# Kernel optimization log

Hardware: AMD Instinct MI355X
Metric: run time of the kernel (lower is better)

Reference implementation:

```python
import jax, jax.numpy as jnp
import numpy as np

NEG_SLOPE = 0.2  # PyG GATConv default leaky_relu slope
EPS = 1e-16


def gat_conv(x, src, dst, W, att_src, att_dst, bias, heads, concat):
    """PyG-style GATConv. x: [N, Fin]; W: [Fin, heads*C]; att_*: [heads, C].
    Edge (src j -> dst i): alpha_ij = softmax_i(leaky_relu(a_src.h_j + a_dst.h_i)).
    """
    N = x.shape[0]
    h = (x @ W).reshape(N, heads, -1)                       # [N, H, C]
    a_s = jnp.einsum('nhc,hc->nh', h, att_src)              # [N, H]
    a_d = jnp.einsum('nhc,hc->nh', h, att_dst)              # [N, H]
    e = jax.nn.leaky_relu(a_s[src] + a_d[dst], NEG_SLOPE)   # [E, H]
    # numerically stable segment softmax over incoming edges of each dst node
    e_max = jax.ops.segment_max(e, dst, num_segments=N)     # [N, H]
    e_max = jnp.where(jnp.isfinite(e_max), e_max, 0.0)      # isolated nodes
    ex = jnp.exp(e - e_max[dst])                            # [E, H]
    denom = jax.ops.segment_sum(ex, dst, num_segments=N)    # [N, H]
    alpha = ex / (denom[dst] + EPS)                         # [E, H]
    msg = alpha[:, :, None] * h[src]                        # [E, H, C]
    out = jax.ops.segment_sum(msg, dst, num_segments=N)     # [N, H, C]
    out = out.reshape(N, -1) if concat else out.mean(axis=1)
    return out + bias


def setup_inputs() -> dict:
    key = jax.random.key(0)
    ks = jax.random.split(key, 12)
    N, E = 100000, 1600000
    Fin, hidden, heads, Fout = 128, 128, 8, 64
    C1 = hidden // heads  # 16
    s = lambda f: 1.0 / np.sqrt(f)
    x = jax.random.normal(ks[0], (N, Fin), dtype=jnp.float32)
    edge_index = jax.random.randint(ks[1], (2, E), 0, N, dtype=jnp.int64)
    W1 = jax.random.normal(ks[2], (Fin, heads * C1), dtype=jnp.float32) * s(Fin)
    att_src1 = jax.random.normal(ks[3], (heads, C1), dtype=jnp.float32) * s(C1)
    att_dst1 = jax.random.normal(ks[4], (heads, C1), dtype=jnp.float32) * s(C1)
    b1 = jnp.zeros((hidden,), dtype=jnp.float32)
    W2 = jax.random.normal(ks[5], (hidden, Fout), dtype=jnp.float32) * s(hidden)
    att_src2 = jax.random.normal(ks[6], (1, Fout), dtype=jnp.float32) * s(Fout)
    att_dst2 = jax.random.normal(ks[7], (1, Fout), dtype=jnp.float32) * s(Fout)
    b2 = jnp.zeros((Fout,), dtype=jnp.float32)
    return {"x": x, "edge_index": edge_index,
            "W1": W1, "att_src1": att_src1, "att_dst1": att_dst1, "b1": b1,
            "W2": W2, "att_src2": att_src2, "att_dst2": att_dst2, "b2": b2}


def reference(x, edge_index, W1, att_src1, att_dst1, b1, W2, att_src2, att_dst2, b2):
    # eval mode: dropouts are identity
    src, dst = edge_index[0], edge_index[1]
    h = gat_conv(x, src, dst, W1, att_src1, att_dst1, b1, heads=8, concat=True)
    h = jax.nn.elu(h)
    out = gat_conv(h, src, dst, W2, att_src2, att_dst2, b2, heads=1, concat=False)
    return out
```

## Files before the change

### kernel.cpp

```cpp
#include <hip/hip_runtime.h>
#include <hip/hip_bf16.h>
#include <hip/hip_fp16.h>
#include <stdint.h>

#define SLOPE 0.2f
#define EPSV 1e-16f
#define LOG2E 1.44269504f
#define H1W 72
#define H2W 36

#define NPB2  256
#define NBLK  512

typedef __attribute__((ext_vector_type(8))) short bf16x8;
typedef __attribute__((ext_vector_type(4))) float f32x4;

static __device__ __forceinline__ uint32_t cvtpk(float a, float b) {
    uint32_t r;
    asm("v_cvt_pk_bf16_f32 %0, %1, %2" : "=v"(r) : "v"(a), "v"(b));
    return r;
}
static __device__ __forceinline__ float lof(uint32_t u) { return __uint_as_float(u << 16); }
static __device__ __forceinline__ float hif(uint32_t u) { return __uint_as_float(u & 0xffff0000u); }

static __device__ __forceinline__ uint32_t pkf16(float a, float b) {
    auto r = __builtin_amdgcn_cvt_pkrtz(a, b);
    return __builtin_bit_cast(uint32_t, r);
}

static __device__ __forceinline__ void fmix_lo(float& acc, uint32_t h2, float w) {
    asm("v_fma_mix_f32 %0, %1, %2, %0 op_sel_hi:[1,0,0]" : "+v"(acc) : "v"(h2), "v"(w));
}
static __device__ __forceinline__ void fmix_hi(float& acc, uint32_t h2, float w) {
    asm("v_fma_mix_f32 %0, %1, %2, %0 op_sel:[1,0,0] op_sel_hi:[1,0,0]" : "+v"(acc) : "v"(h2), "v"(w));
}

union FragCvt { uint4 u; bf16x8 f; };

__global__ __launch_bounds__(256) void prep_kernel(
    const float* __restrict__ W1, const float* __restrict__ W2,
    uint32_t* __restrict__ wt1hi, uint32_t* __restrict__ wt1lo,
    uint32_t* __restrict__ wt2hi, uint32_t* __restrict__ wt2lo)
{
    int t = threadIdx.x;
    if (blockIdx.x == 0) {
        for (int i = t; i < 128 * 64; i += 256) {
            int n = i >> 6, kp = i & 63;
            float w0 = W1[(2 * kp) * 128 + n], w1 = W1[(2 * kp + 1) * 128 + n];
            uint32_t h = cvtpk(w0, w1);
            wt1hi[n * 64 + kp] = h;
            wt1lo[n * 64 + kp] = cvtpk(w0 - lof(h), w1 - hif(h));
        }
    } else {
        for (int i = t; i < 64 * 64; i += 256) {
            int n = i >> 6, kp = i & 63;
            float w0 = W2[(2 * kp) * 64 + n], w1 = W2[(2 * kp + 1) * 64 + n];
            uint32_t h = cvtpk(w0, w1);
            wt2hi[n * 64 + kp] = h;
            wt2lo[n * 64 + kp] = cvtpk(w0 - lof(h), w1 - hif(h));
        }
    }
}

__global__ __launch_bounds__(256) void gemm1_mfma(
    const float* __restrict__ x,
    const uint32_t* __restrict__ wthi, const uint32_t* __restrict__ wtlo,
    const float* __restrict__ att_src, const float* __restrict__ att_dst,
    uint32_t* __restrict__ h1p, float* __restrict__ ad1, int N)
{
    __shared__ uint32_t lds[2][128 * 36];
    const int t = threadIdx.x;
    const int w = t >> 6, l = t & 63;
    const int cl = l & 15, rg = l >> 4;
    const int rowbase = blockIdx.x * 128 + w * 32;

    f32x4 zero = {0.f, 0.f, 0.f, 0.f};
    f32x4 acc[2][8];
    #pragma unroll
    for (int rt = 0; rt < 2; ++rt)
        #pragma unroll
        for (int tl = 0; tl < 8; ++tl) acc[rt][tl] = zero;

    for (int kh = 0; kh < 2; ++kh) {
        if (kh) __syncthreads();
        for (int i = t; i < 1024; i += 256) {
            int col = i >> 3, q = i & 7;
            *(uint4*)&lds[0][col * 36 + q * 4] = *(const uint4*)&wthi[col * 64 + kh * 32 + q * 4];
            *(uint4*)&lds[1][col * 36 + q * 4] = *(const uint4*)&wtlo[col * 64 + kh * 32 + q * 4];
        }
        __syncthreads();
        #pragma unroll
        for (int ks = 0; ks < 2; ++ks) {
            const int kg = kh * 64 + ks * 32 + rg * 8;
            bf16x8 ahi[2], alo[2];
            #pragma unroll
            for (int rt = 0; rt < 2; ++rt) {
                int row = rowbase + rt * 16 + cl;
                row = min(row, N - 1);
                const float* xr = x + (size_t)row * 128 + kg;
                float4 v0 = *(const float4*)xr;
                float4 v1 = *(const float4*)(xr + 4);
                uint32_t h0 = cvtpk(v0.x, v0.y), h1 = cvtpk(v0.z, v0.w);
                uint32_t h2 = cvtpk(v1.x, v1.y), h3 = cvtpk(v1.z, v1.w);
                uint32_t l0 = cvtpk(v0.x - lof(h0), v0.y - hif(h0));
                uint32_t l1 = cvtpk(v0.z - lof(h1), v0.w - hif(h1));
                uint32_t l2 = cvtpk(v1.x - lof(h2), v1.y - hif(h2));
                uint32_t l3 = cvtpk(v1.z - lof(h3), v1.w - hif(h3));
                FragCvt ch, clo;
                ch.u  = make_uint4(h0, h1, h2, h3);
                clo.u = make_uint4(l0, l1, l2, l3);
                ahi[rt] = ch.f; alo[rt] = clo.f;
            }
            #pragma unroll
            for (int tl = 0; tl < 8; ++tl) {
                const int off = (tl * 16 + cl) * 36 + ks * 16 + rg * 4;
                bf16x8 bhi = *(const bf16x8*)&lds[0][off];
                bf16x8 blo = *(const bf16x8*)&lds[1][off];
                #pragma unroll
                for (int rt = 0; rt < 2; ++rt) {
                    acc[rt][tl] = __builtin_amdgcn_mfma_f32_16x16x32_bf16(alo[rt], bhi, acc[rt][tl], 0, 0, 0);
                    acc[rt][tl] = __builtin_amdgcn_mfma_f32_16x16x32_bf16(ahi[rt], blo, acc[rt][tl], 0, 0, 0);
                    acc[rt][tl] = __builtin_amdgcn_mfma_f32_16x16x32_bf16(ahi[rt], bhi, acc[rt][tl], 0, 0, 0);
                }
            }
        }
    }

    #pragma unroll
    for (int rt = 0; rt < 2; ++rt) {
        const int rowb = rowbase + rt * 16 + rg * 4;
        #pragma unroll
        for (int tl = 0; tl < 8; ++tl) {
            f32x4 a = acc[rt][tl];
            float as_ = att_src[tl * 16 + cl] * LOG2E, ad_ = att_dst[tl * 16 + cl] * LOG2E;
            float s0 = a.x * as_, s1 = a.y * as_, s2 = a.z * as_, s3 = a.w * as_;
            float d0 = a.x * ad_, d1 = a.y * ad_, d2 = a.z * ad_, d3 = a.w * ad_;
            #pragma unroll
            for (int off = 1; off < 16; off <<= 1) {
                s0 += __shfl_xor(s0, off); s1 += __shfl_xor(s1, off);
                s2 += __shfl_xor(s2, off); s3 += __shfl_xor(s3, off);
                d0 += __shfl_xor(d0, off); d1 += __shfl_xor(d1, off);
                d2 += __shfl_xor(d2, off); d3 += __shfl_xor(d3, off);
            }
            float av[4] = {a.x, a.y, a.z, a.w};
            #pragma unroll
            for (int r = 0; r < 4; ++r) {
                float partner = __shfl_xor(av[r], 1);
                if (!(cl & 1)) {
                    int row = rowb + r;
                    if (row < N)
                        h1p[(size_t)row * H1W + tl * 8 + (cl >> 1)] = pkf16(av[r], partner);
                }
            }
            if (cl == 0) {
                float sv[4] = {s0, s1, s2, s3}, dv[4] = {d0, d1, d2, d3};
                #pragma unroll
                for (int r = 0; r < 4; ++r) {
                    int row = rowb + r;
                    if (row < N) {
                        h1p[(size_t)row * H1W + 64 + tl] = __float_as_uint(sv[r]);
                        ad1[row * 8 + tl] = dv[r];
                    }
                }
            }
        }
    }
}

__global__ __launch_bounds__(256) void gemm2_mfma(
    const float* __restrict__ h,
    const uint32_t* __restrict__ wthi, const uint32_t* __restrict__ wtlo,
    const float* __restrict__ att_src, const float* __restrict__ att_dst,
    uint32_t* __restrict__ h2p, float* __restrict__ ad2, int N)
{
    __shared__ uint32_t lds[2][64 * 36];
    const int t = threadIdx.x;
    const int w = t >> 6, l = t & 63;
    const int cl = l & 15, rg = l >> 4;
    const int rowbase = blockIdx.x * 128 + w * 32;

    f32x4 zero = {0.f, 0.f, 0.f, 0.f};
    f32x4 acc[2][4];
    #pragma unroll
    for (int rt = 0; rt < 2; ++rt)
        #pragma unroll
        for (int tl = 0; tl < 4; ++tl) acc[rt][tl] = zero;

    for (int kh = 0; kh < 2; ++kh) {
        if (kh) __syncthreads();
        for (int i = t; i < 512; i += 256) {
            int col = i >> 3, q = i & 7;
            *(uint4*)&lds[0][col * 36 + q * 4] = *(const uint4*)&wthi[col * 64 + kh * 32 + q * 4];
            *(uint4*)&lds[1][col * 36 + q * 4] = *(const uint4*)&wtlo[col * 64 + kh * 32 + q * 4];
        }
        __syncthreads();
        #pragma unroll
        for (int ks = 0; ks < 2; ++ks) {
            const int kg = kh * 64 + ks * 32 + rg * 8;
            bf16x8 ahi[2], alo[2];
            #pragma unroll
            for (int rt = 0; rt < 2; ++rt) {
                int row = rowbase + rt * 16 + cl;
                row = min(row, N - 1);
                const float* xr = h + (size_t)row * 128 + kg;
                float4 v0 = *(const float4*)xr;
                float4 v1 = *(const float4*)(xr + 4);
                uint32_t h0 = cvtpk(v0.x, v0.y), h1 = cvtpk(v0.z, v0.w);
                uint32_t h2 = cvtpk(v1.x, v1.y), h3 = cvtpk(v1.z, v1.w);
                uint32_t l0 = cvtpk(v0.x - lof(h0), v0.y - hif(h0));
                uint32_t l1 = cvtpk(v0.z - lof(h1), v0.w - hif(h1));
                uint32_t l2 = cvtpk(v1.x - lof(h2), v1.y - hif(h2));
                uint32_t l3 = cvtpk(v1.z - lof(h3), v1.w - hif(h3));
                FragCvt ch, clo;
                ch.u  = make_uint4(h0, h1, h2, h3);
                clo.u = make_uint4(l0, l1, l2, l3);
                ahi[rt] = ch.f; alo[rt] = clo.f;
            }
            #pragma unroll
            for (int tl = 0; tl < 4; ++tl) {
                const int off = (tl * 16 + cl) * 36 + ks * 16 + rg * 4;
                bf16x8 bhi = *(const bf16x8*)&lds[0][off];
                bf16x8 blo = *(const bf16x8*)&lds[1][off];
                #pragma unroll
                for (int rt = 0; rt < 2; ++rt) {
                    acc[rt][tl] = __builtin_amdgcn_mfma_f32_16x16x32_bf16(alo[rt], bhi, acc[rt][tl], 0, 0, 0);
                    acc[rt][tl] = __builtin_amdgcn_mfma_f32_16x16x32_bf16(ahi[rt], blo, acc[rt][tl], 0, 0, 0);
                    acc[rt][tl] = __builtin_amdgcn_mfma_f32_16x16x32_bf16(ahi[rt], bhi, acc[rt][tl], 0, 0, 0);
                }
            }
        }
    }

    #pragma unroll
    for (int rt = 0; rt < 2; ++rt) {
        const int rowb = rowbase + rt * 16 + rg * 4;
        float s0 = 0.f, s1 = 0.f, s2 = 0.f, s3 = 0.f;
        float d0 = 0.f, d1 = 0.f, d2 = 0.f, d3 = 0.f;
        #pragma unroll
        for (int tl = 0; tl < 4; ++tl) {
            f32x4 a = acc[rt][tl];
            float as_ = att_src[tl * 16 + cl] * LOG2E, ad_ = att_dst[tl * 16 + cl] * LOG2E;
            s0 += a.x * as_; s1 += a.y * as_; s2 += a.z * as_; s3 += a.w * as_;
            d0 += a.x * ad_; d1 += a.y * ad_; d2 += a.z * ad_; d3 += a.w * ad_;
            float av[4] = {a.x, a.y, a.z, a.w};
            #pragma unroll
            for (int r = 0; r < 4; ++r) {
                float partner = __shfl_xor(av[r], 1);
                if (!(cl & 1)) {
                    int row = rowb + r;
                    if (row < N)
                        h2p[(size_t)row * H2W + tl * 8 + (cl >> 1)] = pkf16(av[r], partner);
                }
            }
        }
        #pragma unroll
        for (int off = 1; off < 16; off <<= 1) {
            s0 += __shfl_xor(s0, off); s1 += __shfl_xor(s1, off);
            s2 += __shfl_xor(s2, off); s3 += __shfl_xor(s3, off);
            d0 += __shfl_xor(d0, off); d1 += __shfl_xor(d1, off);
            d2 += __shfl_xor(d2, off); d3 += __shfl_xor(d3, off);
        }
        if (cl == 0) {
            float sv[4] = {s0, s1, s2, s3}, dv[4] = {d0, d1, d2, d3};
            #pragma unroll
            for (int r = 0; r < 4; ++r) {
                int row = rowb + r;
                if (row < N) {
                    h2p[(size_t)row * H2W + 32] = __float_as_uint(sv[r]);
                    ad2[row] = dv[r];
                }
            }
        }
    }
}

__global__ __launch_bounds__(256) void s_count(
    const int* __restrict__ ei, int* __restrict__ pbh, int E, int NB, int chunk)
{
    __shared__ int hist[512];
    int t = threadIdx.x;
    hist[t] = 0; hist[t + 256] = 0;
    __syncthreads();
    int e0 = blockIdx.x * chunk, e1 = min(E, e0 + chunk);
    for (int e = e0 + t; e < e1; e += 256)
        atomicAdd(&hist[ei[E + e] >> 8], 1);
    __syncthreads();
    for (int b = t; b < NB; b += 256)
        pbh[(size_t)b * NBLK + blockIdx.x] = hist[b];
}

__global__ __launch_bounds__(256) void s_scanA(
    const int* __restrict__ pbh, int* __restrict__ btot, int NB)
{
    __shared__ int red[256];
    int b = blockIdx.x, t = threadIdx.x;
    int s = pbh[(size_t)b * NBLK + t] + pbh[(size_t)b * NBLK + 256 + t];
    red[t] = s; __syncthreads();
    for (int off = 128; off; off >>= 1) {
        if (t < off) red[t] += red[t + off];
        __syncthreads();
    }
    if (t == 0) btot[b] = red[0];
}

__global__ __launch_bounds__(512) void s_scanB(
    const int* __restrict__ btot, int* __restrict__ bucket_base, int NB, int E)
{
    __shared__ int sc[512];
    int t = threadIdx.x;
    int v = (t < NB) ? btot[t] : 0;
    sc[t] = v; __syncthreads();
    for (int off = 1; off < 512; off <<= 1) {
        int add = (t >= off) ? sc[t - off] : 0;
        __syncthreads();
        sc[t] += add;
        __syncthreads();
    }
    if (t < NB) bucket_base[t] = sc[t] - v;
    if (t == 0) bucket_base[NB] = E;
}

__global__ __launch_bounds__(256) void s_scanC(
    int* __restrict__ pbh, const int* __restrict__ bucket_base, int NB)
{
    __shared__ int ps[256];
    int b = blockIdx.x, t = threadIdx.x;
    int v0 = pbh[(size_t)b * NBLK + 2 * t], v1 = pbh[(size_t)b * NBLK + 2 * t + 1];
    int p = v0 + v1;
    ps[t] = p; __syncthreads();
    for (int off = 1; off < 256; off <<= 1) {
        int add = (t >= off) ? ps[t - off] : 0;
        __syncthreads();
        ps[t] += add;
        __syncthreads();
    }
    int ex = bucket_base[b] + ps[t] - p;
    pbh[(size_t)b * NBLK + 2 * t]     = ex;
    pbh[(size_t)b * NBLK + 2 * t + 1] = ex + v0;
}

__global__ __launch_bounds__(256) void s_place(
    const int* __restrict__ ei, const int* __restrict__ pbh,
    uint32_t* __restrict__ staging, int E, int NB, int chunk)
{
    __shared__ int lcur[512];
    int t = threadIdx.x;
    if (t < NB)       lcur[t]       = pbh[(size_t)t * NBLK + blockIdx.x];
    if (t + 256 < NB) lcur[t + 256] = pbh[(size_t)(t + 256) * NBLK + blockIdx.x];
    __syncthreads();
    int e0 = blockIdx.x * chunk, e1 = min(E, e0 + chunk);
    for (int e = e0 + t; e < e1; e += 256) {
        int s = ei[e], d = ei[E + e];
        int p = atomicAdd(&lcur[d >> 8], 1);
        staging[p] = ((uint32_t)s << 8) | (uint32_t)(d & 255);
    }
}

__global__ __launch_bounds__(256) void s_build(
    const uint32_t* __restrict__ staging, const int* __restrict__ bucket_base,
    int* __restrict__ row_start, int* __restrict__ sorted_src, int N, int E, int NB)
{
    __shared__ int cnt[256];
    __shared__ int ofs[256];
    __shared__ int ps[256];
    int b = blockIdx.x, t = threadIdx.x;
    int base = bucket_base[b], end = bucket_base[b + 1];
    cnt[t] = 0;
    __syncthreads();
    for (int i = base + t; i < end; i += 256)
        atomicAdd(&cnt[staging[i] & 255], 1);
    __syncthreads();
    int c = cnt[t];
    ps[t] = c; __syncthreads();
    for (int off = 1; off < 256; off <<= 1) {
        int add = (t >= off) ? ps[t - off] : 0;
        __syncthreads();
        ps[t] += add;
        __syncthreads();
    }
    int ex = ps[t] - c;
    ofs[t] = ex;
    int node = b * NPB2 + t;
    if (node < N) row_start[node] = base + ex;
    if (b == NB - 1 && t == 0) row_start[N] = E;
    __syncthreads();
    for (int i = base + t; i < end; i += 256) {
        uint32_t v = staging[i];
        int pos = base + atomicAdd(&ofs[v & 255], 1);
        sorted_src[pos] = (int)(v >> 8);
    }
}

__global__ __launch_bounds__(256) void gather1_kernel(
    const int* __restrict__ row_start, const int* __restrict__ sorted_src,
    const float* __restrict__ ad1, const uint32_t* __restrict__ h1p,
    const float* __restrict__ b1, float* __restrict__ hbuf, int N)
{
    int node = blockIdx.x * 4 + (threadIdx.x >> 6);
    if (node >= N) return;
    const int l  = threadIdx.x & 63;
    const int wh = l & 7;
    const int eA = l >> 3;
    const int c8 = l & 15;
    const int q  = l >> 4;
    const int hB = c8 >> 1;

    int r0 = row_start[node], r1 = row_start[node + 1];

    if (r0 == r1) {
        if (l < 16) {
            #pragma unroll
            for (int g = 0; g < 2; ++g) {
                float4 bv = *(const float4*)&b1[c8 * 8 + g * 4];
                bv.x = bv.x > 0.f ? bv.x : expm1f(bv.x);
                bv.y = bv.y > 0.f ? bv.y : expm1f(bv.y);
                bv.z = bv.z > 0.f ? bv.z : expm1f(bv.z);
                bv.w = bv.w > 0.f ? bv.w : expm1f(bv.w);
                *(float4*)&hbuf[(size_t)node * 128 + c8 * 8 + g * 4] = bv;
            }
        }
        return;
    }

    float adw = ad1[node * 8 + wh];
    const uint32_t* rowp = h1p + 4 * c8;
    float acc[8] = {0.f, 0.f, 0.f, 0.f, 0.f, 0.f, 0.f, 0.f};
    float den = 0.f;

    int jw = r0 + eA;
    int sw0 = sorted_src[jw < r1 ? jw : r0] * H1W;
    int j1 = r0 + 8 + eA;
    int sw1 = sorted_src[j1 < r1 ? j1 : r0] * H1W;
    float av0 = __uint_as_float(h1p[sw0 + 64 + wh]);

    for (int j = r0; j < r1; j += 8) {
        int jn = j + 16 + eA;
        int swn = sorted_src[jn < r1 ? jn : r0] * H1W;
        float avn = __uint_as_float(h1p[sw1 + 64 + wh]);

        float ev = av0 + adw;
        ev = ev > 0.f ? ev : SLOPE * ev;
        float w = (j + eA) < r1 ? exp2f(ev) : 0.f;
        den += w;

        #pragma unroll
        for (int k = 0; k < 2; ++k) {
            int eidx = q + 4 * k;
            float wk  = __shfl(w,   eidx * 8 + hB, 64);
            int   ofk = __shfl(sw0, eidx * 8,      64);
            uint4 hv = *(const uint4*)(rowp + ofk);
            fmix_lo(acc[0], hv.x, wk); fmix_hi(acc[1], hv.x, wk);
            fmix_lo(acc[2], hv.y, wk); fmix_hi(acc[3], hv.y, wk);
            fmix_lo(acc[4], hv.z, wk); fmix_hi(acc[5], hv.z, wk);
            fmix_lo(acc[6], hv.w, wk); fmix_hi(acc[7], hv.w, wk);
        }
        sw0 = sw1; sw1 = swn; av0 = avn;
    }

    den += __shfl_xor(den, 8, 64);
    den += __shfl_xor(den, 16, 64);
    den += __shfl_xor(den, 32, 64);
    float dB = __shfl(den, hB, 64);

    #pragma unroll
    for (int i = 0; i < 8; ++i) {
        acc[i] += __shfl_xor(acc[i], 16, 64);
        acc[i] += __shfl_xor(acc[i], 32, 64);
    }

    if (l < 16) {
        float inv = 1.0f / (dB + EPSV);
        #pragma unroll
        for (int g = 0; g < 2; ++g) {
            float4 bv = *(const float4*)&b1[c8 * 8 + g * 4];
            float v0 = acc[g * 4 + 0] * inv + bv.x;
            float v1 = acc[g * 4 + 1] * inv + bv.y;
            float v2 = acc[g * 4 + 2] * inv + bv.z;
            float v3 = acc[g * 4 + 3] * inv + bv.w;
            v0 = v0 > 0.f ? v0 : expm1f(v0);
            v1 = v1 > 0.f ? v1 : expm1f(v1);
            v2 = v2 > 0.f ? v2 : expm1f(v2);
            v3 = v3 > 0.f ? v3 : expm1f(v3);
            *(float4*)&hbuf[(size_t)node * 128 + c8 * 8 + g * 4] = make_float4(v0, v1, v2, v3);
        }
    }
}

__global__ __launch_bounds__(256) void gather2_kernel(
    const int* __restrict__ row_start, const int* __restrict__ sorted_src,
    const float* __restrict__ ad2, const uint32_t* __restrict__ h2p,
    const float* __restrict__ b2, float* __restrict__ out, int N)
{
    int node = blockIdx.x * 8 + (threadIdx.x >> 5);
    if (node >= N) return;
    const int l  = threadIdx.x & 31;
    const int eA = l & 7;
    const int c8 = l & 7;
    const int q  = l >> 3;

    int r0 = row_start[node], r1 = row_start[node + 1];

    if (r0 == r1) {
        if (l < 8) {
            #pragma unroll
            for (int g = 0; g < 2; ++g) {
                float4 bv = *(const float4*)&b2[c8 * 8 + g * 4];
                *(float4*)&out[(size_t)node * 64 + c8 * 8 + g * 4] = bv;
            }
        }
        return;
    }

    float ad = ad2[node];
    const uint32_t* rowp = h2p + 4 * c8;
    float acc[8] = {0.f, 0.f, 0.f, 0.f, 0.f, 0.f, 0.f, 0.f};
    float den = 0.f;

    int jw = r0 + eA;
    int sw0 = sorted_src[jw < r1 ? jw : r0] * H2W;
    int j1 = r0 + 8 + eA;
    int sw1 = sorted_src[j1 < r1 ? j1 : r0] * H2W;
    float av0 = __uint_as_float(h2p[sw0 + 32]);

    for (int j = r0; j < r1; j += 8) {
        int jn = j + 16 + eA;
        int swn = sorted_src[jn < r1 ? jn : r0] * H2W;
        float avn = __uint_as_float(h2p[sw1 + 32]);

        float ev = av0 + ad;
        ev = ev > 0.f ? ev : SLOPE * ev;
        float w = (j + eA) < r1 ? exp2f(ev) : 0.f;
        den += w;

        #pragma unroll
        for (int k = 0; k < 2; ++k) {
            int eidx = q + 4 * k;
            float wk  = __shfl(w,   eidx, 32);
            int   ofk = __shfl(sw0, eidx, 32);
            uint4 hv = *(const uint4*)(rowp + ofk);
            fmix_lo(acc[0], hv.x, wk); fmix_hi(acc[1], hv.x, wk);
            fmix_lo(acc[2], hv.y, wk); fmix_hi(acc[3], hv.y, wk);
            fmix_lo(acc[4], hv.z, wk); fmix_hi(acc[5], hv.z, wk);
            fmix_lo(acc[6], hv.w, wk); fmix_hi(acc[7], hv.w, wk);
        }
        sw0 = sw1; sw1 = swn; av0 = avn;
    }

    den += __shfl_xor(den, 1, 32);
    den += __shfl_xor(den, 2, 32);
    den += __shfl_xor(den, 4, 32);
    #pragma unroll
    for (int i = 0; i < 8; ++i) {
        acc[i] += __shfl_xor(acc[i], 8, 32);
        acc[i] += __shfl_xor(acc[i], 16, 32);
    }

    if (l < 8) {
        float inv = 1.0f / (den + EPSV);
        #pragma unroll
        for (int g = 0; g < 2; ++g) {
            float4 bv = *(const float4*)&b2[c8 * 8 + g * 4];
            *(float4*)&out[(size_t)node * 64 + c8 * 8 + g * 4] =
                make_float4(acc[g * 4 + 0] * inv + bv.x, acc[g * 4 + 1] * inv + bv.y,
                            acc[g * 4 + 2] * inv + bv.z, acc[g * 4 + 3] * inv + bv.w);
        }
    }
}

extern "C" void kernel_launch(void* const* d_in, const int* in_sizes, int n_in,
                              void* d_out, int out_size, void* d_ws, size_t ws_size,
                              hipStream_t stream)
{
    const int N = in_sizes[0] / 128;
    const int E = in_sizes[1] / 2;
    const int NB = (N + NPB2 - 1) / NPB2;
    const int chunk = (E + NBLK - 1) / NBLK;

    const float* x        = (const float*)d_in[0];
    const int*   ei       = (const int*)  d_in[1];
    const float* W1       = (const float*)d_in[2];
    const float* att_src1 = (const float*)d_in[3];
    const float* att_dst1 = (const float*)d_in[4];
    const float* b1       = (const float*)d_in[5];
    const float* W2       = (const float*)d_in[6];
    const float* att_src2 = (const float*)d_in[7];
    const float* att_dst2 = (const float*)d_in[8];
    const float* b2       = (const float*)d_in[9];
    float* out = (float*)d_out;

    uint32_t* h1p  = (uint32_t*)d_ws;
    float* hbuf    = (float*)(h1p + (size_t)N * H1W);
    float* ad1     = hbuf + (size_t)N * 128;
    float* ad2     = ad1  + (size_t)N * 8;
    int* row_start   = (int*)(ad2 + N);
    int* bucket_base = row_start + (N + 1);
    int* btot        = bucket_base + (NB + 1);
    int* pbh         = btot + NB;
    int* sorted_src  = pbh + (size_t)NB * NBLK;
    uint32_t* staging = (uint32_t*)(sorted_src + E);
    uint32_t* wt1hi = staging + E;
    uint32_t* wt1lo = wt1hi + 128 * 64;
    uint32_t* wt2hi = wt1lo + 128 * 64;
    uint32_t* wt2lo = wt2hi + 64 * 64;
    uint32_t* h2p   = h1p;

    prep_kernel<<<2, 256, 0, stream>>>(W1, W2, wt1hi, wt1lo, wt2hi, wt2lo);

    s_count<<<NBLK, 256, 0, stream>>>(ei, pbh, E, NB, chunk);
    s_scanA<<<NB, 256, 0, stream>>>(pbh, btot, NB);
    s_scanB<<<1, 512, 0, stream>>>(btot, bucket_base, NB, E);
    s_scanC<<<NB, 256, 0, stream>>>(pbh, bucket_base, NB);
    s_place<<<NBLK, 256, 0, stream>>>(ei, pbh, staging, E, NB, chunk);
    s_build<<<NB, 256, 0, stream>>>(staging, bucket_base, row_start, sorted_src, N, E, NB);

    gemm1_mfma<<<(N + 127) / 128, 256, 0, stream>>>(x, wt1hi, wt1lo, att_src1, att_dst1, h1p, ad1, N);
    gather1_kernel<<<(N + 3) / 4, 256, 0, stream>>>(row_start, sorted_src, ad1, h1p, b1, hbuf, N);

    gemm2_mfma<<<(N + 127) / 128, 256, 0, stream>>>(hbuf, wt2hi, wt2lo, att_src2, att_dst2, h2p, ad2, N);
    gather2_kernel<<<(N + 7) / 8, 256, 0, stream>>>(row_start, sorted_src, ad2, h2p, b2, out, N);
}
```

Before: 257.9 us.

## Fold weight prep and bucket scan into neighbours; software-pipeline gather row loads

Merges the weight-split prep kernel into s_count as two extra blocks and folds the single-block bucket scan into s_scanC, where each block recomputes the global prefix over bucket totals. Together these remove two kernel launches and their serialization gaps. Both gather kernels now issue the h-row loads for the next 8-edge group one iteration ahead, so gather latency overlaps the FMA work. The cost is redundant scan work in every s_scanC block and more registers held live in the gather loops.

```diff
diff --git a/kernel.cpp b/kernel.cpp
--- a/kernel.cpp
+++ b/kernel.cpp
@@ -36,31 +36,6 @@
 }
 
 union FragCvt { uint4 u; bf16x8 f; };
-
-__global__ __launch_bounds__(256) void prep_kernel(
-    const float* __restrict__ W1, const float* __restrict__ W2,
-    uint32_t* __restrict__ wt1hi, uint32_t* __restrict__ wt1lo,
-    uint32_t* __restrict__ wt2hi, uint32_t* __restrict__ wt2lo)
-{
-    int t = threadIdx.x;
-    if (blockIdx.x == 0) {
-        for (int i = t; i < 128 * 64; i += 256) {
-            int n = i >> 6, kp = i & 63;
-            float w0 = W1[(2 * kp) * 128 + n], w1 = W1[(2 * kp + 1) * 128 + n];
-            uint32_t h = cvtpk(w0, w1);
-            wt1hi[n * 64 + kp] = h;
-            wt1lo[n * 64 + kp] = cvtpk(w0 - lof(h), w1 - hif(h));
-        }
-    } else {
-        for (int i = t; i < 64 * 64; i += 256) {
-            int n = i >> 6, kp = i & 63;
-            float w0 = W2[(2 * kp) * 64 + n], w1 = W2[(2 * kp + 1) * 64 + n];
-            uint32_t h = cvtpk(w0, w1);
-            wt2hi[n * 64 + kp] = h;
-            wt2lo[n * 64 + kp] = cvtpk(w0 - lof(h), w1 - hif(h));
-        }
-    }
-}
 
 __global__ __launch_bounds__(256) void gemm1_mfma(
     const float* __restrict__ x,
@@ -275,10 +250,33 @@
 }
 
 __global__ __launch_bounds__(256) void s_count(
-    const int* __restrict__ ei, int* __restrict__ pbh, int E, int NB, int chunk)
-{
+    const int* __restrict__ ei, int* __restrict__ pbh, int E, int NB, int chunk,
+    const float* __restrict__ W1, const float* __restrict__ W2,
+    uint32_t* __restrict__ wt1hi, uint32_t* __restrict__ wt1lo,
+    uint32_t* __restrict__ wt2hi, uint32_t* __restrict__ wt2lo)
+{
+    int t = threadIdx.x;
+    if (blockIdx.x >= NBLK) {
+        if (blockIdx.x == NBLK) {
+            for (int i = t; i < 128 * 64; i += 256) {
+                int n = i >> 6, kp = i & 63;
+                float w0 = W1[(2 * kp) * 128 + n], w1 = W1[(2 * kp + 1) * 128 + n];
+                uint32_t h = cvtpk(w0, w1);
+                wt1hi[n * 64 + kp] = h;
+                wt1lo[n * 64 + kp] = cvtpk(w0 - lof(h), w1 - hif(h));
+            }
+        } else {
+            for (int i = t; i < 64 * 64; i += 256) {
+                int n = i >> 6, kp = i & 63;
+                float w0 = W2[(2 * kp) * 64 + n], w1 = W2[(2 * kp + 1) * 64 + n];
+                uint32_t h = cvtpk(w0, w1);
+                wt2hi[n * 64 + kp] = h;
+                wt2lo[n * 64 + kp] = cvtpk(w0 - lof(h), w1 - hif(h));
+            }
+        }
+        return;
+    }
     __shared__ int hist[512];
-    int t = threadIdx.x;
     hist[t] = 0; hist[t + 256] = 0;
     __syncthreads();
     int e0 = blockIdx.x * chunk, e1 = min(E, e0 + chunk);
@@ -303,29 +301,15 @@
     if (t == 0) btot[b] = red[0];
 }
 
-__global__ __launch_bounds__(512) void s_scanB(
-    const int* __restrict__ btot, int* __restrict__ bucket_base, int NB, int E)
-{
-    __shared__ int sc[512];
-    int t = threadIdx.x;
-    int v = (t < NB) ? btot[t] : 0;
-    sc[t] = v; __syncthreads();
-    for (int off = 1; off < 512; off <<= 1) {
-        int add = (t >= off) ? sc[t - off] : 0;
-        __syncthreads();
-        sc[t] += add;
-        __syncthreads();
-    }
-    if (t < NB) bucket_base[t] = sc[t] - v;
-    if (t == 0) bucket_base[NB] = E;
-}
-
 __global__ __launch_bounds__(256) void s_scanC(
-    int* __restrict__ pbh, const int* __restrict__ bucket_base, int NB)
+    int* __restrict__ pbh, const int* __restrict__ btot,
+    int* __restrict__ bucket_base, int NB, int E)
 {
     __shared__ int ps[256];
+    __shared__ int exv[512];
     int b = blockIdx.x, t = threadIdx.x;
-    int v0 = pbh[(size_t)b * NBLK + 2 * t], v1 = pbh[(size_t)b * NBLK + 2 * t + 1];
+    int v0 = (2 * t     < NB) ? btot[2 * t]     : 0;
+    int v1 = (2 * t + 1 < NB) ? btot[2 * t + 1] : 0;
     int p = v0 + v1;
     ps[t] = p; __syncthreads();
     for (int off = 1; off < 256; off <<= 1) {
@@ -334,9 +318,27 @@
         ps[t] += add;
         __syncthreads();
     }
-    int ex = bucket_base[b] + ps[t] - p;
+    int pex = ps[t] - p;
+    exv[2 * t] = pex; exv[2 * t + 1] = pex + v0;
+    __syncthreads();
+    int base = exv[b];
+    if (t == 0) {
+        bucket_base[b] = base;
+        if (b == NB - 1) bucket_base[NB] = E;
+    }
+    __syncthreads();
+    int w0 = pbh[(size_t)b * NBLK + 2 * t], w1 = pbh[(size_t)b * NBLK + 2 * t + 1];
+    int pp = w0 + w1;
+    ps[t] = pp; __syncthreads();
+    for (int off = 1; off < 256; off <<= 1) {
+        int add = (t >= off) ? ps[t - off] : 0;
+        __syncthreads();
+        ps[t] += add;
+        __syncthreads();
+    }
+    int ex = base + ps[t] - pp;
     pbh[(size_t)b * NBLK + 2 * t]     = ex;
-    pbh[(size_t)b * NBLK + 2 * t + 1] = ex + v0;
+    pbh[(size_t)b * NBLK + 2 * t + 1] = ex + w0;
 }
 
 __global__ __launch_bounds__(256) void s_place(
@@ -433,27 +435,38 @@
     int sw1 = sorted_src[j1 < r1 ? j1 : r0] * H1W;
     float av0 = __uint_as_float(h1p[sw0 + 64 + wh]);
 
+    int of0A = __shfl(sw0,  q      * 8, 64);
+    int of1A = __shfl(sw0, (q + 4) * 8, 64);
+    uint4 hA0 = *(const uint4*)(rowp + of0A);
+    uint4 hA1 = *(const uint4*)(rowp + of1A);
+
     for (int j = r0; j < r1; j += 8) {
         int jn = j + 16 + eA;
         int swn = sorted_src[jn < r1 ? jn : r0] * H1W;
         float avn = __uint_as_float(h1p[sw1 + 64 + wh]);
 
+        int of0B = __shfl(sw1,  q      * 8, 64);
+        int of1B = __shfl(sw1, (q + 4) * 8, 64);
+        uint4 hB0 = *(const uint4*)(rowp + of0B);
+        uint4 hB1 = *(const uint4*)(rowp + of1B);
+
         float ev = av0 + adw;
         ev = ev > 0.f ? ev : SLOPE * ev;
         float w = (j + eA) < r1 ? exp2f(ev) : 0.f;
         den += w;
 
-        #pragma unroll
-        for (int k = 0; k < 2; ++k) {
-            int eidx = q + 4 * k;
-            float wk  = __shfl(w,   eidx * 8 + hB, 64);
-            int   ofk = __shfl(sw0, eidx * 8,      64);
-            uint4 hv = *(const uint4*)(rowp + ofk);
-            fmix_lo(acc[0], hv.x, wk); fmix_hi(acc[1], hv.x, wk);
-            fmix_lo(acc[2], hv.y, wk); fmix_hi(acc[3], hv.y, wk);
-            fmix_lo(acc[4], hv.z, wk); fmix_hi(acc[5], hv.z, wk);
-            fmix_lo(acc[6], hv.w, wk); fmix_hi(acc[7], hv.w, wk);
-        }
+        float wk0 = __shfl(w,  q      * 8 + hB, 64);
+        float wk1 = __shfl(w, (q + 4) * 8 + hB, 64);
+        fmix_lo(acc[0], hA0.x, wk0); fmix_hi(acc[1], hA0.x, wk0);
+        fmix_lo(acc[2], hA0.y, wk0); fmix_hi(acc[3], hA0.y, wk0);
+        fmix_lo(acc[4], hA0.z, wk0); fmix_hi(acc[5], hA0.z, wk0);
+        fmix_lo(acc[6], hA0.w, wk0); fmix_hi(acc[7], hA0.w, wk0);
+        fmix_lo(acc[0], hA1.x, wk1); fmix_hi(acc[1], hA1.x, wk1);
+        fmix_lo(acc[2], hA1.y, wk1); fmix_hi(acc[3], hA1.y, wk1);
+        fmix_lo(acc[4], hA1.z, wk1); fmix_hi(acc[5], hA1.z, wk1);
+        fmix_lo(acc[6], hA1.w, wk1); fmix_hi(acc[7], hA1.w, wk1);
+
+        hA0 = hB0; hA1 = hB1;
         sw0 = sw1; sw1 = swn; av0 = avn;
     }
 
@@ -522,27 +535,38 @@
     int sw1 = sorted_src[j1 < r1 ? j1 : r0] * H2W;
     float av0 = __uint_as_float(h2p[sw0 + 32]);
 
+    int of0A = __shfl(sw0, q,     32);
+    int of1A = __shfl(sw0, q + 4, 32);
+    uint4 hA0 = *(const uint4*)(rowp + of0A);
+    uint4 hA1 = *(const uint4*)(rowp + of1A);
+
     for (int j = r0; j < r1; j += 8) {
         int jn = j + 16 + eA;
         int swn = sorted_src[jn < r1 ? jn : r0] * H2W;
         float avn = __uint_as_float(h2p[sw1 + 32]);
 
+        int of0B = __shfl(sw1, q,     32);
+        int of1B = __shfl(sw1, q + 4, 32);
+        uint4 hB0 = *(const uint4*)(rowp + of0B);
+        uint4 hB1 = *(const uint4*)(rowp + of1B);
+
         float ev = av0 + ad;
         ev = ev > 0.f ? ev : SLOPE * ev;
         float w = (j + eA) < r1 ? exp2f(ev) : 0.f;
         den += w;
 
-        #pragma unroll
-        for (int k = 0; k < 2; ++k) {
-            int eidx = q + 4 * k;
-            float wk  = __shfl(w,   eidx, 32);
-            int   ofk = __shfl(sw0, eidx, 32);
-            uint4 hv = *(const uint4*)(rowp + ofk);
-            fmix_lo(acc[0], hv.x, wk); fmix_hi(acc[1], hv.x, wk);
-            fmix_lo(acc[2], hv.y, wk); fmix_hi(acc[3], hv.y, wk);
-            fmix_lo(acc[4], hv.z, wk); fmix_hi(acc[5], hv.z, wk);
-            fmix_lo(acc[6], hv.w, wk); fmix_hi(acc[7], hv.w, wk);
-        }
+        float wk0 = __shfl(w, q,     32);
+        float wk1 = __shfl(w, q + 4, 32);
+        fmix_lo(acc[0], hA0.x, wk0); fmix_hi(acc[1], hA0.x, wk0);
+        fmix_lo(acc[2], hA0.y, wk0); fmix_hi(acc[3], hA0.y, wk0);
+        fmix_lo(acc[4], hA0.z, wk0); fmix_hi(acc[5], hA0.z, wk0);
+        fmix_lo(acc[6], hA0.w, wk0); fmix_hi(acc[7], hA0.w, wk0);
+        fmix_lo(acc[0], hA1.x, wk1); fmix_hi(acc[1], hA1.x, wk1);
+        fmix_lo(acc[2], hA1.y, wk1); fmix_hi(acc[3], hA1.y, wk1);
+        fmix_lo(acc[4], hA1.z, wk1); fmix_hi(acc[5], hA1.z, wk1);
+        fmix_lo(acc[6], hA1.w, wk1); fmix_hi(acc[7], hA1.w, wk1);
+
+        hA0 = hB0; hA1 = hB1;
         sw0 = sw1; sw1 = swn; av0 = avn;
     }
 
@@ -604,12 +628,10 @@
     uint32_t* wt2lo = wt2hi + 64 * 64;
     uint32_t* h2p   = h1p;
 
-    prep_kernel<<<2, 256, 0, stream>>>(W1, W2, wt1hi, wt1lo, wt2hi, wt2lo);
-
-    s_count<<<NBLK, 256, 0, stream>>>(ei, pbh, E, NB, chunk);
+    s_count<<<NBLK + 2, 256, 0, stream>>>(ei, pbh, E, NB, chunk,
+                                          W1, W2, wt1hi, wt1lo, wt2hi, wt2lo);
     s_scanA<<<NB, 256, 0, stream>>>(pbh, btot, NB);
-    s_scanB<<<1, 512, 0, stream>>>(btot, bucket_base, NB, E);
-    s_scanC<<<NB, 256, 0, stream>>>(pbh, bucket_base, NB);
+    s_scanC<<<NB, 256, 0, stream>>>(pbh, btot, bucket_base, NB, E);
     s_place<<<NBLK, 256, 0, stream>>>(ei, pbh, staging, E, NB, chunk);
     s_build<<<NB, 256, 0, stream>>>(staging, bucket_base, row_start, sorted_src, N, E, NB);
 
```

Result: faster. 249.4 us (median of 2 runs) (-3.3%).
